# Optimization experiments

Hardware: AMD Instinct MI355X
Metric: run time of the kernel (lower is better)

Reference implementation:

```python
import jax, jax.numpy as jnp
import numpy as np

D_MODEL = 256
D_STATE = 64
R_MIN, R_MAX, MAX_PHASE = 0.0, 1.0, 6.28


def setup_inputs() -> dict:
    key = jax.random.key(0)
    ks = jax.random.split(key, 8)
    u1 = jax.random.uniform(ks[0], (D_STATE,), dtype=jnp.float32)
    u2 = jax.random.uniform(ks[1], (D_STATE,), dtype=jnp.float32)
    nu_log = jnp.log(-0.5 * jnp.log(u1 * (R_MAX**2 - R_MIN**2) + R_MIN**2))
    theta_log = jnp.log(u2 * MAX_PHASE)
    sB = 1.0 / np.sqrt(2 * D_STATE)
    sC = 1.0 / np.sqrt(D_STATE)
    B_re = jax.random.normal(ks[2], (D_MODEL, D_STATE), dtype=jnp.float32) * sB
    B_im = jax.random.normal(ks[3], (D_MODEL, D_STATE), dtype=jnp.float32) * sB
    C_re = jax.random.normal(ks[4], (D_MODEL, D_STATE), dtype=jnp.float32) * sC
    C_im = jax.random.normal(ks[5], (D_MODEL, D_STATE), dtype=jnp.float32) * sC
    D = jax.random.normal(ks[6], (D_MODEL,), dtype=jnp.float32)
    x = jax.random.normal(ks[7], (4, 8192, D_MODEL), dtype=jnp.float32)
    return {"x": x, "nu_log": nu_log, "theta_log": theta_log,
            "B_re": B_re, "B_im": B_im, "C_re": C_re, "C_im": C_im, "D": D}


def reference(x, nu_log, theta_log, B_re, B_im, C_re, C_im, D):
    B, L, H = x.shape
    # diagonal transition: Lambda = exp(-exp(nu) + i*exp(theta)); Lambda^k = exp(k*log_lambda)
    log_lambda = -jnp.exp(nu_log) + 1j * jnp.exp(theta_log)          # (n,)
    k = jnp.arange(L, dtype=jnp.float32)
    Lambda_k = jnp.exp(k[:, None] * log_lambda[None, :])              # (L, n) complex
    CB = (C_re + 1j * C_im) * (B_re + 1j * B_im)                      # (H, n)
    kernels = jnp.einsum('hn,ln->hl', CB, Lambda_k).real              # (H, L)
    # FFT (causal, linear) convolution per channel
    n_fft = 2 * L
    x_f = jnp.fft.rfft(x, n=n_fft, axis=1)                            # (B, L+1, H)
    k_f = jnp.fft.rfft(kernels, n=n_fft, axis=1)                      # (H, L+1)
    y_f = x_f * k_f.T[None]                                           # (B, L+1, H)
    y = jnp.fft.irfft(y_f, n=n_fft, axis=1)[:, :L, :]
    return y + x * D[None, None, :]
```

## Files before the change

kernel.cpp:

```cpp
#include <hip/hip_runtime.h>
#include <hip/hip_bf16.h>

#define BB   4
#define LL   8192
#define HH   256
#define NN   64
#define NSEG 128
#define LSEG 64

typedef __attribute__((ext_vector_type(8))) short  short8;
typedef __attribute__((ext_vector_type(4))) float  float4v;
typedef __attribute__((ext_vector_type(4))) int    int4v;


__device__ __forceinline__ float ldF(const void* p, size_t i, int isbf) {
    return isbf ? __bfloat162float(((const __hip_bfloat16*)p)[i])
                : ((const float*)p)[i];
}

__device__ __forceinline__ unsigned int packbf(float re, float im) {
    __hip_bfloat16 hr = __float2bfloat16(re);
    __hip_bfloat16 hi = __float2bfloat16(im);
    return ((unsigned int)*(unsigned short*)&hi << 16)
         |  (unsigned int)*(unsigned short*)&hr;
}
__device__ __forceinline__ float unpkre(unsigned int u) {
    unsigned short s = (unsigned short)(u & 0xFFFFu);
    return __bfloat162float(*(__hip_bfloat16*)&s);
}
__device__ __forceinline__ float unpkim(unsigned int u) {
    unsigned short s = (unsigned short)(u >> 16);
    return __bfloat162float(*(__hip_bfloat16*)&s);
}

__global__ void k_sniff(const void* p0, const void* p1, const void* p2,
                        const void* p3, const void* p4, const void* p5,
                        const void* p6, const void* p7, int* flags)
{
    int t = threadIdx.x;
    if (t < 8) {
        const void* ps[8] = {p0, p1, p2, p3, p4, p5, p6, p7};
        const unsigned int* d = (const unsigned int*)ps[t];
        int nbf = 0, nrand = 0;
        for (int i = 0; i < 32; ++i) {
            unsigned int lo = d[i] & 0xFFFFu;
            unsigned int e  = (lo >> 7) & 0xFFu;
            if (lo == 0u) {  }
            else if (e >= 90u && e <= 140u) nbf++;
            else nrand++;
        }
        flags[t] = (nrand == 0 && nbf >= 8) ? 1 : 0;
    }
}

__global__ __launch_bounds__(256) void k_setup(
    const void* nu_log, const void* theta_log,
    const void* B_re, const void* B_im,
    const void* C_re, const void* C_im,
    const void* D, const int* __restrict__ flags,
    float* lam, float* lam64, float* Df, float* CBt,
    float* PsegRe, float* PsegIm)
{
    int t = blockIdx.x * 256 + threadIdx.x;
    if (t < NN) {
        float nu = expf(ldF(nu_log, t, flags[1]));
        float th = expf(ldF(theta_log, t, flags[2]));
        float a  = expf(-nu);
        lam[2*t]   = a * cosf(th);
        lam[2*t+1] = a * sinf(th);
        float a64 = expf(-64.0f * nu);
        float ph  = 64.0f * th;
        lam64[2*t]   = a64 * cosf(ph);
        lam64[2*t+1] = a64 * sinf(ph);
    }
    if (t < HH) Df[t] = ldF(D, t, flags[7]);
    if (t < HH * NN) {
        int h = t >> 6, n = t & 63;
        float bre = ldF(B_re, h*NN+n, flags[3]);
        float bim = ldF(B_im, h*NN+n, flags[4]);
        float cre = ldF(C_re, h*NN+n, flags[5]);
        float cim = ldF(C_im, h*NN+n, flags[6]);
        CBt[(n*2+0)*HH + h] = cre*bre - cim*bim;
        CBt[(n*2+1)*HH + h] = cre*bim + cim*bre;
    }
    if (t < 64 * 64) {
        int l = t >> 6, n = t & 63;
        float nu = expf(ldF(nu_log, n, flags[1]));
        float th = expf(ldF(theta_log, n, flags[2]));
        float fp = (float)(63 - l);
        float ar = expf(-fp * nu);
        PsegRe[t] = ar * cosf(fp * th);
        PsegIm[t] = ar * sinf(fp * th);
    }
}

__global__ __launch_bounds__(256) void k_ktab(
    const float* __restrict__ CBt, const float* __restrict__ PsegRe,
    const float* __restrict__ PsegIm, const float* __restrict__ lam64,
    float* __restrict__ Ktab,
    short* __restrict__ VreT, short* __restrict__ VimnT,
    short* __restrict__ PreH, short* __restrict__ PreL,
    short* __restrict__ PimH, short* __restrict__ PimL)
{
    int t = blockIdx.x * 256 + threadIdx.x;
    int h = t >> 6, j = t & 63;
    float acc = 0.f;
    for (int n = 0; n < NN; ++n)
        acc += CBt[(2*n)*HH + h]   * PsegRe[(63-j)*64 + n]
             - CBt[(2*n+1)*HH + h] * PsegIm[(63-j)*64 + n];
    Ktab[j*HH + h] = acc;
    if (t < 64*64) {
        int tau = t >> 6, n = t & 63;
        float vr, vi;
        if (tau < 63) {
            vr =  PsegRe[(62-tau)*64 + n];
            vi = -PsegIm[(62-tau)*64 + n];
        } else {
            vr =  lam64[2*n];
            vi = -lam64[2*n+1];
        }
        __hip_bfloat16 br = __float2bfloat16(vr);
        __hip_bfloat16 bi = __float2bfloat16(vi);
        VreT[tau*64 + n]  = *(short*)&br;
        VimnT[tau*64 + n] = *(short*)&bi;

        int n2 = t >> 6, l2 = t & 63;
        float pr = PsegRe[l2*64 + n2];
        float pi = PsegIm[l2*64 + n2];
        __hip_bfloat16 prh = __float2bfloat16(pr);
        __hip_bfloat16 prl = __float2bfloat16(pr - __bfloat162float(prh));
        __hip_bfloat16 pih = __float2bfloat16(pi);
        __hip_bfloat16 pil = __float2bfloat16(pi - __bfloat162float(pih));
        PreH[t] = *(short*)&prh;
        PreL[t] = *(short*)&prl;
        PimH[t] = *(short*)&pih;
        PimL[t] = *(short*)&pil;
    }
}

template<bool ISBF>
__device__ __forceinline__ void segsum_body(
    const void* __restrict__ x, size_t xbase,
    const short* __restrict__ PreH, const short* __restrict__ PreL,
    const short* __restrict__ PimH, const short* __restrict__ PimL,
    unsigned int* __restrict__ Apack, size_t abase, int q, int l15)
{
    #pragma unroll
    for (int nt = 0; nt < 4; ++nt) {
        short8 xh[2], xl[2];
        #pragma unroll
        for (int ks = 0; ks < 2; ++ks)
            #pragma unroll
            for (int j = 0; j < 8; ++j) {
                size_t a = xbase + nt*16 + (size_t)(ks*32 + q*8 + j)*HH;
                if (ISBF) {
                    xh[ks][j] = ((const short*)x)[a];
                } else {
                    float xf = ((const float*)x)[a];
                    __hip_bfloat16 hv = __float2bfloat16(xf);
                    __hip_bfloat16 lv = __float2bfloat16(xf - __bfloat162float(hv));
                    xh[ks][j] = *(short*)&hv;
                    xl[ks][j] = *(short*)&lv;
                }
            }
        #pragma unroll
        for (int mt = 0; mt < 4; ++mt) {
            float4v ar = {0.f, 0.f, 0.f, 0.f};
            float4v ai = {0.f, 0.f, 0.f, 0.f};
            #pragma unroll
            for (int ks = 0; ks < 2; ++ks) {
                int off = (mt*16 + l15)*64 + ks*32 + q*8;
                short8 prh = *(const short8*)(PreH + off);
                short8 pih = *(const short8*)(PimH + off);
                short8 prl = *(const short8*)(PreL + off);
                short8 pil = *(const short8*)(PimL + off);
                ar = __builtin_amdgcn_mfma_f32_16x16x32_bf16(prh, xh[ks], ar, 0, 0, 0);
                ai = __builtin_amdgcn_mfma_f32_16x16x32_bf16(pih, xh[ks], ai, 0, 0, 0);
                ar = __builtin_amdgcn_mfma_f32_16x16x32_bf16(prl, xh[ks], ar, 0, 0, 0);
                ai = __builtin_amdgcn_mfma_f32_16x16x32_bf16(pil, xh[ks], ai, 0, 0, 0);
                if (!ISBF) {
                    ar = __builtin_amdgcn_mfma_f32_16x16x32_bf16(prh, xl[ks], ar, 0, 0, 0);
                    ai = __builtin_amdgcn_mfma_f32_16x16x32_bf16(pih, xl[ks], ai, 0, 0, 0);
                }
            }
            #pragma unroll
            for (int r = 0; r < 4; ++r) {
                int n = mt*16 + q*4 + r;
                Apack[abase + (size_t)n*64 + nt*16 + l15] = packbf(ar[r], ai[r]);
            }
        }
    }
}

__global__ __launch_bounds__(256) void k_segsum(
    const void* __restrict__ x,
    const short* __restrict__ PreH, const short* __restrict__ PreL,
    const short* __restrict__ PimH, const short* __restrict__ PimL,
    const int* __restrict__ flags, unsigned int* __restrict__ Apack)
{
    int bk = blockIdx.x;
    int s  = bk & (NSEG - 1);
    int b  = bk >> 7;
    int w    = threadIdx.x >> 6;
    int lane = threadIdx.x & 63;
    int q = lane >> 4, l15 = lane & 15;

    size_t xbase = ((size_t)(b*LL) + s*64) * HH + w*64 + l15;
    size_t abase = (((size_t)(b*4 + w) * NSEG + s) * NN) * 64;

    if (flags[0]) segsum_body<true >(x, xbase, PreH, PreL, PimH, PimL, Apack, abase, q, l15);
    else          segsum_body<false>(x, xbase, PreH, PreL, PimH, PimL, Apack, abase, q, l15);
}

__global__ __launch_bounds__(256) void k_scan(
    const float* __restrict__ lam64, const float* __restrict__ CBt,
    unsigned int* __restrict__ Apack)
{
    int w    = blockIdx.x * 4 + (threadIdx.x >> 6);
    int lane = threadIdx.x & 63;
    int n    = w & 63;
    int hg   = (w >> 6) & 3;
    int b    = w >> 8;
    int h    = hg*64 + lane;

    float lre = lam64[2*n], lim = lam64[2*n+1];
    float cbre = CBt[(2*n)*HH + h], cbim = CBt[(2*n+1)*HH + h];
    float sre = 0.f, sim = 0.f;
    size_t base0 = (((size_t)(b*4 + hg) * NSEG) * NN + n) * 64 + lane;

    unsigned int curU[16], nxtU[16];
    #pragma unroll
    for (int k = 0; k < 16; ++k)
        curU[k] = Apack[base0 + (size_t)k * NN * 64];
    #pragma unroll
    for (int blk = 0; blk < 8; ++blk) {
        if (blk < 7) {
            #pragma unroll
            for (int k = 0; k < 16; ++k)
                nxtU[k] = Apack[base0 + (size_t)((blk+1)*16 + k) * NN * 64];
        }
        #pragma unroll
        for (int k = 0; k < 16; ++k) {
            size_t idx = base0 + (size_t)(blk*16 + k) * NN * 64;
            float are = unpkre(curU[k]);
            float aim = unpkim(curU[k]);
            float ure = cbre*sre - cbim*sim;
            float uim = cbre*sim + cbim*sre;
            Apack[idx] = packbf(ure, uim);
            float t2 = fmaf(lre, sre, fmaf(-lim, sim, are));
            sim = fmaf(lre, sim, fmaf(lim, sre, aim));
            sre = t2;
        }
        #pragma unroll
        for (int k = 0; k < 16; ++k) curU[k] = nxtU[k];
    }
}

template<bool ISBF, int U>
__device__ __forceinline__ void conv_u(
    const void* __restrict__ x, const float* __restrict__ Df,
    const float* __restrict__ Ktab, const short* __restrict__ xs,
    const float* __restrict__ yc,
    int b, int s, int h, float* __restrict__ y)
{
    int g0 = s*64 + U*16;
    size_t rbase = ((size_t)b*LL + g0)*HH + h;
    float xv[16], yv[16];
    float dh = Df[h];
    #pragma unroll
    for (int t = 0; t < 16; ++t) {
        float xl;
        if (ISBF) xl = __bfloat162float(((const __hip_bfloat16*)x)[rbase + (size_t)t*HH]);
        else      xl = ((const float*)x)[rbase + (size_t)t*HH];
        xv[t] = xl;
        yv[t] = fmaf(dh, xl, yc[(U*16 + t)*HH + h]);
    }
    float kreg[16*U + 16];
    #pragma unroll
    for (int j = 0; j < 16*U + 16; ++j) kreg[j] = Ktab[j*HH + h];
    #pragma unroll
    for (int j = 0; j < 16; ++j)
        #pragma unroll
        for (int t = j; t < 16; ++t) yv[t] = fmaf(kreg[j], xv[t-j], yv[t]);
    #pragma unroll
    for (int m = 0; m < 16*U; ++m) {
        short bits = xs[(U*16 - 1 - m)*HH + h];
        float xm = __bfloat162float(*(const __hip_bfloat16*)&bits);
        #pragma unroll
        for (int t = 0; t < 16; ++t) yv[t] = fmaf(kreg[t+1+m], xm, yv[t]);
    }
    #pragma unroll
    for (int t = 0; t < 16; ++t) y[rbase + (size_t)t*HH] = yv[t];
}

template<bool ISBF>
__device__ __forceinline__ void cc_body(
    const short* __restrict__ VreT, const short* __restrict__ VimnT,
    const unsigned int* __restrict__ Upack, const void* __restrict__ x,
    const float* __restrict__ Df, const float* __restrict__ Ktab,
    float* yc, short* xs, int b, int s, float* __restrict__ y)
{
    int t = threadIdx.x;

    size_t sb = ((size_t)b*LL + s*64) * HH;
    if (ISBF) {
        const int4v* xp = (const int4v*)((const __hip_bfloat16*)x + sb);
        int4v* xd = (int4v*)xs;
        xd[t]        = xp[t];
        xd[t + 1024] = xp[t + 1024];
    } else {
        const float* xp = (const float*)x + sb;
        #pragma unroll
        for (int i = 0; i < 2; ++i) {
            int e = (t + i*1024) * 8;
            #pragma unroll
            for (int j = 0; j < 8; ++j) {
                __hip_bfloat16 v = __float2bfloat16(xp[e + j]);
                xs[e + j] = *(short*)&v;
            }
        }
    }

    int w = t >> 6, lane = t & 63;
    int hg = w & 3, nt = w >> 2;
    int q = lane >> 4, l15 = lane & 15;
    size_t ubase = (((size_t)(b*4 + hg) * NSEG + s) * NN) * 64;

    int l = nt*16 + l15;
    short8 bre[2], bim[2];
    #pragma unroll
    for (int ks = 0; ks < 2; ++ks)
        #pragma unroll
        for (int j = 0; j < 8; ++j) {
            int n = ks*32 + q*8 + j;
            unsigned int u = Upack[ubase + (size_t)n*64 + l];
            bre[ks][j] = (short)(u & 0xFFFFu);
            bim[ks][j] = (short)(u >> 16);
        }
    int h = hg*64 + l;
    #pragma unroll
    for (int mt = 0; mt < 4; ++mt) {
        float4v acc = {0.f, 0.f, 0.f, 0.f};
        #pragma unroll
        for (int ks = 0; ks < 2; ++ks) {
            int off = (mt*16 + l15)*64 + ks*32 + q*8;
            short8 afr = *(const short8*)(VreT + off);
            short8 afi = *(const short8*)(VimnT + off);
            acc = __builtin_amdgcn_mfma_f32_16x16x32_bf16(afr, bre[ks], acc, 0, 0, 0);
            acc = __builtin_amdgcn_mfma_f32_16x16x32_bf16(afi, bim[ks], acc, 0, 0, 0);
        }
        #pragma unroll
        for (int r = 0; r < 4; ++r) {
            int tau = mt*16 + q*4 + r;
            yc[tau*HH + h] = acc[r];
        }
    }

    __syncthreads();

    int u = w >> 2;
    int h2 = hg*64 + lane;
    switch (u) {
        case 0: conv_u<ISBF,0>(x, Df, Ktab, xs, yc, b, s, h2, y); break;
        case 1: conv_u<ISBF,1>(x, Df, Ktab, xs, yc, b, s, h2, y); break;
        case 2: conv_u<ISBF,2>(x, Df, Ktab, xs, yc, b, s, h2, y); break;
        case 3: conv_u<ISBF,3>(x, Df, Ktab, xs, yc, b, s, h2, y); break;
    }
}

__global__ __launch_bounds__(1024) void k_cc(
    const short* __restrict__ VreT, const short* __restrict__ VimnT,
    const unsigned int* __restrict__ Upack, const void* __restrict__ x,
    const float* __restrict__ Df, const float* __restrict__ Ktab,
    const int* __restrict__ flags, float* __restrict__ y)
{
    __shared__ float yc[64 * HH];
    __shared__ short xs[64 * HH];
    int bk = blockIdx.x;
    int s  = bk & (NSEG - 1);
    int b  = bk >> 7;
    if (flags[0]) cc_body<true >(VreT, VimnT, Upack, x, Df, Ktab, yc, xs, b, s, y);
    else          cc_body<false>(VreT, VimnT, Upack, x, Df, Ktab, yc, xs, b, s, y);
}

extern "C" void kernel_launch(void* const* d_in, const int* in_sizes, int n_in,
                              void* d_out, int out_size, void* d_ws, size_t ws_size,
                              hipStream_t stream)
{
    const void* x  = d_in[0];
    const void* nu = d_in[1];
    const void* th = d_in[2];
    const void* Br = d_in[3];
    const void* Bi = d_in[4];
    const void* Cr = d_in[5];
    const void* Ci = d_in[6];
    const void* D  = d_in[7];

    char* ws = (char*)d_ws;
    float* lam    = (float*)(ws);
    float* lam64  = (float*)(ws + 512);
    int*   flags  = (int*)(ws + 1024);
    float* Df     = (float*)(ws + 1088);
    float* CBt    = (float*)(ws + 2112);
    float* Ktab   = (float*)(ws + 133184);
    short* VreT   = (short*)(ws + 198720);
    short* VimnT  = (short*)(ws + 206912);
    float* PsegRe = (float*)(ws + 215104);
    float* PsegIm = (float*)(ws + 231744);
    short* PreH   = (short*)(ws + 248128);
    short* PreL   = (short*)(ws + 256320);
    short* PimH   = (short*)(ws + 264512);
    short* PimL   = (short*)(ws + 272704);
    unsigned int* Apack = (unsigned int*)(ws + 294912);
    float* yout = (float*)d_out;

    k_sniff<<<dim3(1), dim3(64), 0, stream>>>(x, nu, th, Br, Bi, Cr, Ci, D, flags);
    k_setup<<<dim3(64), dim3(256), 0, stream>>>(nu, th, Br, Bi, Cr, Ci, D, flags,
                                                lam, lam64, Df, CBt, PsegRe, PsegIm);
    k_ktab<<<dim3(64), dim3(256), 0, stream>>>(CBt, PsegRe, PsegIm, lam64,
                                               Ktab, VreT, VimnT,
                                               PreH, PreL, PimH, PimL);
    k_segsum<<<dim3(512), dim3(256), 0, stream>>>(x, PreH, PreL, PimH, PimL,
                                                  flags, Apack);
    k_scan<<<dim3(256), dim3(256), 0, stream>>>(lam64, CBt, Apack);
    k_cc<<<dim3(512), dim3(1024), 0, stream>>>(VreT, VimnT, Apack,
                                               x, Df, Ktab, flags, yout);
}
```

Measured before the change: 178.9 us.

## Inline dtype sniffing into kernels and split segsum across four column tiles

Drops the separate sniff kernel launch. Each kernel now detects the input dtype itself: k_setup puts the flags in shared memory, and k_segsum and k_cc scan the first 32 words of x per thread. k_segsum moves its nt loop into the grid, going from 512 to 2048 blocks, each handling one 16-column tile, to raise parallelism and shorten each block. The cost is redundant sniff loads in every thread and P-matrix reloads repeated across four times as many blocks.

After: 196.1 us. 1.1x slower.

```diff
diff --git a/kernel.cpp b/kernel.cpp
--- a/kernel.cpp
+++ b/kernel.cpp
@@ -18,6 +18,19 @@
                 : ((const float*)p)[i];
 }
 
+__device__ __forceinline__ int sniff1(const void* p) {
+    const unsigned int* d = (const unsigned int*)p;
+    int nbf = 0, nrand = 0;
+    for (int i = 0; i < 32; ++i) {
+        unsigned int lo = d[i] & 0xFFFFu;
+        unsigned int e  = (lo >> 7) & 0xFFu;
+        if (lo == 0u) {  }
+        else if (e >= 90u && e <= 140u) nbf++;
+        else nrand++;
+    }
+    return (nrand == 0 && nbf >= 8) ? 1 : 0;
+}
+
 __device__ __forceinline__ unsigned int packbf(float re, float im) {
     __hip_bfloat16 hr = __float2bfloat16(re);
     __hip_bfloat16 hi = __float2bfloat16(im);
@@ -33,38 +46,28 @@
     return __bfloat162float(*(__hip_bfloat16*)&s);
 }
 
-__global__ void k_sniff(const void* p0, const void* p1, const void* p2,
-                        const void* p3, const void* p4, const void* p5,
-                        const void* p6, const void* p7, int* flags)
-{
-    int t = threadIdx.x;
-    if (t < 8) {
-        const void* ps[8] = {p0, p1, p2, p3, p4, p5, p6, p7};
-        const unsigned int* d = (const unsigned int*)ps[t];
-        int nbf = 0, nrand = 0;
-        for (int i = 0; i < 32; ++i) {
-            unsigned int lo = d[i] & 0xFFFFu;
-            unsigned int e  = (lo >> 7) & 0xFFu;
-            if (lo == 0u) {  }
-            else if (e >= 90u && e <= 140u) nbf++;
-            else nrand++;
-        }
-        flags[t] = (nrand == 0 && nbf >= 8) ? 1 : 0;
-    }
-}
-
 __global__ __launch_bounds__(256) void k_setup(
     const void* nu_log, const void* theta_log,
     const void* B_re, const void* B_im,
     const void* C_re, const void* C_im,
-    const void* D, const int* __restrict__ flags,
+    const void* D,
     float* lam, float* lam64, float* Df, float* CBt,
     float* PsegRe, float* PsegIm)
 {
+    __shared__ int sf[8];
+    {
+        int tt = threadIdx.x;
+        if (tt >= 1 && tt < 8) {
+            const void* ps[8] = {nullptr, nu_log, theta_log, B_re, B_im,
+                                 C_re, C_im, D};
+            sf[tt] = sniff1(ps[tt]);
+        }
+        __syncthreads();
+    }
     int t = blockIdx.x * 256 + threadIdx.x;
     if (t < NN) {
-        float nu = expf(ldF(nu_log, t, flags[1]));
-        float th = expf(ldF(theta_log, t, flags[2]));
+        float nu = expf(ldF(nu_log, t, sf[1]));
+        float th = expf(ldF(theta_log, t, sf[2]));
         float a  = expf(-nu);
         lam[2*t]   = a * cosf(th);
         lam[2*t+1] = a * sinf(th);
@@ -73,20 +76,20 @@
         lam64[2*t]   = a64 * cosf(ph);
         lam64[2*t+1] = a64 * sinf(ph);
     }
-    if (t < HH) Df[t] = ldF(D, t, flags[7]);
+    if (t < HH) Df[t] = ldF(D, t, sf[7]);
     if (t < HH * NN) {
         int h = t >> 6, n = t & 63;
-        float bre = ldF(B_re, h*NN+n, flags[3]);
-        float bim = ldF(B_im, h*NN+n, flags[4]);
-        float cre = ldF(C_re, h*NN+n, flags[5]);
-        float cim = ldF(C_im, h*NN+n, flags[6]);
+        float bre = ldF(B_re, h*NN+n, sf[3]);
+        float bim = ldF(B_im, h*NN+n, sf[4]);
+        float cre = ldF(C_re, h*NN+n, sf[5]);
+        float cim = ldF(C_im, h*NN+n, sf[6]);
         CBt[(n*2+0)*HH + h] = cre*bre - cim*bim;
         CBt[(n*2+1)*HH + h] = cre*bim + cim*bre;
     }
     if (t < 64 * 64) {
         int l = t >> 6, n = t & 63;
-        float nu = expf(ldF(nu_log, n, flags[1]));
-        float th = expf(ldF(theta_log, n, flags[2]));
+        float nu = expf(ldF(nu_log, n, sf[1]));
+        float th = expf(ldF(theta_log, n, sf[2]));
         float fp = (float)(63 - l);
         float ar = expf(-fp * nu);
         PsegRe[t] = ar * cosf(fp * th);
@@ -145,49 +148,46 @@
     const short* __restrict__ PimH, const short* __restrict__ PimL,
     unsigned int* __restrict__ Apack, size_t abase, int q, int l15)
 {
-    #pragma unroll
-    for (int nt = 0; nt < 4; ++nt) {
-        short8 xh[2], xl[2];
-        #pragma unroll
-        for (int ks = 0; ks < 2; ++ks)
-            #pragma unroll
-            for (int j = 0; j < 8; ++j) {
-                size_t a = xbase + nt*16 + (size_t)(ks*32 + q*8 + j)*HH;
-                if (ISBF) {
-                    xh[ks][j] = ((const short*)x)[a];
-                } else {
-                    float xf = ((const float*)x)[a];
-                    __hip_bfloat16 hv = __float2bfloat16(xf);
-                    __hip_bfloat16 lv = __float2bfloat16(xf - __bfloat162float(hv));
-                    xh[ks][j] = *(short*)&hv;
-                    xl[ks][j] = *(short*)&lv;
-                }
+    short8 xh[2], xl[2];
+    #pragma unroll
+    for (int ks = 0; ks < 2; ++ks)
+        #pragma unroll
+        for (int j = 0; j < 8; ++j) {
+            size_t a = xbase + (size_t)(ks*32 + q*8 + j)*HH;
+            if (ISBF) {
+                xh[ks][j] = ((const short*)x)[a];
+            } else {
+                float xf = ((const float*)x)[a];
+                __hip_bfloat16 hv = __float2bfloat16(xf);
+                __hip_bfloat16 lv = __float2bfloat16(xf - __bfloat162float(hv));
+                xh[ks][j] = *(short*)&hv;
+                xl[ks][j] = *(short*)&lv;
             }
-        #pragma unroll
-        for (int mt = 0; mt < 4; ++mt) {
-            float4v ar = {0.f, 0.f, 0.f, 0.f};
-            float4v ai = {0.f, 0.f, 0.f, 0.f};
-            #pragma unroll
-            for (int ks = 0; ks < 2; ++ks) {
-                int off = (mt*16 + l15)*64 + ks*32 + q*8;
-                short8 prh = *(const short8*)(PreH + off);
-                short8 pih = *(const short8*)(PimH + off);
-                short8 prl = *(const short8*)(PreL + off);
-                short8 pil = *(const short8*)(PimL + off);
-                ar = __builtin_amdgcn_mfma_f32_16x16x32_bf16(prh, xh[ks], ar, 0, 0, 0);
-                ai = __builtin_amdgcn_mfma_f32_16x16x32_bf16(pih, xh[ks], ai, 0, 0, 0);
-                ar = __builtin_amdgcn_mfma_f32_16x16x32_bf16(prl, xh[ks], ar, 0, 0, 0);
-                ai = __builtin_amdgcn_mfma_f32_16x16x32_bf16(pil, xh[ks], ai, 0, 0, 0);
-                if (!ISBF) {
-                    ar = __builtin_amdgcn_mfma_f32_16x16x32_bf16(prh, xl[ks], ar, 0, 0, 0);
-                    ai = __builtin_amdgcn_mfma_f32_16x16x32_bf16(pih, xl[ks], ai, 0, 0, 0);
-                }
+        }
+    #pragma unroll
+    for (int mt = 0; mt < 4; ++mt) {
+        float4v ar = {0.f, 0.f, 0.f, 0.f};
+        float4v ai = {0.f, 0.f, 0.f, 0.f};
+        #pragma unroll
+        for (int ks = 0; ks < 2; ++ks) {
+            int off = (mt*16 + l15)*64 + ks*32 + q*8;
+            short8 prh = *(const short8*)(PreH + off);
+            short8 pih = *(const short8*)(PimH + off);
+            short8 prl = *(const short8*)(PreL + off);
+            short8 pil = *(const short8*)(PimL + off);
+            ar = __builtin_amdgcn_mfma_f32_16x16x32_bf16(prh, xh[ks], ar, 0, 0, 0);
+            ai = __builtin_amdgcn_mfma_f32_16x16x32_bf16(pih, xh[ks], ai, 0, 0, 0);
+            ar = __builtin_amdgcn_mfma_f32_16x16x32_bf16(prl, xh[ks], ar, 0, 0, 0);
+            ai = __builtin_amdgcn_mfma_f32_16x16x32_bf16(pil, xh[ks], ai, 0, 0, 0);
+            if (!ISBF) {
+                ar = __builtin_amdgcn_mfma_f32_16x16x32_bf16(prh, xl[ks], ar, 0, 0, 0);
+                ai = __builtin_amdgcn_mfma_f32_16x16x32_bf16(pih, xl[ks], ai, 0, 0, 0);
             }
-            #pragma unroll
-            for (int r = 0; r < 4; ++r) {
-                int n = mt*16 + q*4 + r;
-                Apack[abase + (size_t)n*64 + nt*16 + l15] = packbf(ar[r], ai[r]);
-            }
+        }
+        #pragma unroll
+        for (int r = 0; r < 4; ++r) {
+            int n = mt*16 + q*4 + r;
+            Apack[abase + (size_t)n*64] = packbf(ar[r], ai[r]);
         }
     }
 }
@@ -196,20 +196,22 @@
     const void* __restrict__ x,
     const short* __restrict__ PreH, const short* __restrict__ PreL,
     const short* __restrict__ PimH, const short* __restrict__ PimL,
-    const int* __restrict__ flags, unsigned int* __restrict__ Apack)
-{
+    unsigned int* __restrict__ Apack)
+{
+    int isbf = sniff1(x);
     int bk = blockIdx.x;
-    int s  = bk & (NSEG - 1);
-    int b  = bk >> 7;
+    int nt = bk & 3;
+    int s  = (bk >> 2) & (NSEG - 1);
+    int b  = bk >> 9;
     int w    = threadIdx.x >> 6;
     int lane = threadIdx.x & 63;
     int q = lane >> 4, l15 = lane & 15;
 
-    size_t xbase = ((size_t)(b*LL) + s*64) * HH + w*64 + l15;
-    size_t abase = (((size_t)(b*4 + w) * NSEG + s) * NN) * 64;
-
-    if (flags[0]) segsum_body<true >(x, xbase, PreH, PreL, PimH, PimL, Apack, abase, q, l15);
-    else          segsum_body<false>(x, xbase, PreH, PreL, PimH, PimL, Apack, abase, q, l15);
+    size_t xbase = ((size_t)(b*LL) + s*64) * HH + w*64 + nt*16 + l15;
+    size_t abase = (((size_t)(b*4 + w) * NSEG + s) * NN) * 64 + nt*16 + l15;
+
+    if (isbf) segsum_body<true >(x, xbase, PreH, PreL, PimH, PimL, Apack, abase, q, l15);
+    else      segsum_body<false>(x, xbase, PreH, PreL, PimH, PimL, Apack, abase, q, l15);
 }
 
 __global__ __launch_bounds__(256) void k_scan(
@@ -372,15 +374,16 @@
     const short* __restrict__ VreT, const short* __restrict__ VimnT,
     const unsigned int* __restrict__ Upack, const void* __restrict__ x,
     const float* __restrict__ Df, const float* __restrict__ Ktab,
-    const int* __restrict__ flags, float* __restrict__ y)
+    float* __restrict__ y)
 {
     __shared__ float yc[64 * HH];
     __shared__ short xs[64 * HH];
+    int isbf = sniff1(x);
     int bk = blockIdx.x;
     int s  = bk & (NSEG - 1);
     int b  = bk >> 7;
-    if (flags[0]) cc_body<true >(VreT, VimnT, Upack, x, Df, Ktab, yc, xs, b, s, y);
-    else          cc_body<false>(VreT, VimnT, Upack, x, Df, Ktab, yc, xs, b, s, y);
+    if (isbf) cc_body<true >(VreT, VimnT, Upack, x, Df, Ktab, yc, xs, b, s, y);
+    else      cc_body<false>(VreT, VimnT, Upack, x, Df, Ktab, yc, xs, b, s, y);
 }
 
 extern "C" void kernel_launch(void* const* d_in, const int* in_sizes, int n_in,
@@ -399,7 +402,6 @@
     char* ws = (char*)d_ws;
     float* lam    = (float*)(ws);
     float* lam64  = (float*)(ws + 512);
-    int*   flags  = (int*)(ws + 1024);
     float* Df     = (float*)(ws + 1088);
     float* CBt    = (float*)(ws + 2112);
     float* Ktab   = (float*)(ws + 133184);
@@ -414,15 +416,14 @@
     unsigned int* Apack = (unsigned int*)(ws + 294912);
     float* yout = (float*)d_out;
 
-    k_sniff<<<dim3(1), dim3(64), 0, stream>>>(x, nu, th, Br, Bi, Cr, Ci, D, flags);
-    k_setup<<<dim3(64), dim3(256), 0, stream>>>(nu, th, Br, Bi, Cr, Ci, D, flags,
+    k_setup<<<dim3(64), dim3(256), 0, stream>>>(nu, th, Br, Bi, Cr, Ci, D,
                                                 lam, lam64, Df, CBt, PsegRe, PsegIm);
     k_ktab<<<dim3(64), dim3(256), 0, stream>>>(CBt, PsegRe, PsegIm, lam64,
                                                Ktab, VreT, VimnT,
                                                PreH, PreL, PimH, PimL);
-    k_segsum<<<dim3(512), dim3(256), 0, stream>>>(x, PreH, PreL, PimH, PimL,
-                                                  flags, Apack);
+    k_segsum<<<dim3(2048), dim3(256), 0, stream>>>(x, PreH, PreL, PimH, PimL,
+                                                   Apack);
     k_scan<<<dim3(256), dim3(256), 0, stream>>>(lam64, CBt, Apack);
     k_cc<<<dim3(512), dim3(1024), 0, stream>>>(VreT, VimnT, Apack,
-                                               x, Df, Ktab, flags, yout);
-}
+                                               x, Df, Ktab, yout);
+}
```
